# Optimization experiments

Measured on AMD Instinct MI355X. Metric: run time of the kernel, lower is better.

## Reference

```python
import jax, jax.numpy as jnp
import numpy as np

N_NODES = 100000   # total atoms across batch
N_EDGES = 1600000  # directed edges (avg degree 16)
ATOM_FDIM = 75
N_MOLS = 1024
DEPTH = 3


def setup_inputs() -> dict:
    key = jax.random.key(0)
    ks = jax.random.split(key, 8)
    h = jax.random.normal(ks[0], (N_NODES, ATOM_FDIM), dtype=jnp.float32)
    # U: Linear(2*atom_fdim -> atom_fdim); NN: Linear(atom_fdim -> 1)
    U_w = jax.random.normal(ks[1], (ATOM_FDIM, 2 * ATOM_FDIM), dtype=jnp.float32) * (1.0 / np.sqrt(2 * ATOM_FDIM))
    U_b = jnp.zeros((ATOM_FDIM,), dtype=jnp.float32)
    NN_w = jax.random.normal(ks[2], (1, ATOM_FDIM), dtype=jnp.float32) * (1.0 / np.sqrt(ATOM_FDIM))
    NN_b = jnp.zeros((1,), dtype=jnp.float32)
    edge_src = jax.random.randint(ks[3], (N_EDGES,), 0, N_NODES, dtype=jnp.int32)
    edge_dst = jax.random.randint(ks[4], (N_EDGES,), 0, N_NODES, dtype=jnp.int32)
    mol_id = jnp.sort(jax.random.randint(ks[5], (N_NODES,), 0, N_MOLS, dtype=jnp.int32))
    return {
        "h": h, "U_w": U_w, "U_b": U_b, "NN_w": NN_w, "NN_b": NN_b,
        "edge_src": edge_src, "edge_dst": edge_dst, "mol_id": mol_id,
        "depth": DEPTH, "num_mols": N_MOLS,
    }


def reference(h, U_w, U_b, NN_w, NN_b, edge_src, edge_dst, mol_id, depth, num_mols):
    n_nodes = h.shape[0]
    for _ in range(depth):
        # message: sum of neighbor atom features (gather + scatter-add)
        m = jax.ops.segment_sum(h[edge_src], edge_dst, num_segments=n_nodes)  # [N, D]
        # update: h_v = relu(U([h_v ; m_v]))
        h = jax.nn.relu(jnp.concatenate([h, m], axis=-1) @ U_w.T + U_b)
    # readout: sum atom vectors per molecule, then Linear(D -> 1)
    mol_vec = jax.ops.segment_sum(h, mol_id, num_segments=num_mols)  # [B, D]
    out = mol_vec @ NN_w.T + NN_b  # [B, 1]
    return out
```

## Files before the change

kernel.cpp:

```cpp
#include <hip/hip_runtime.h>

#define FDIM 75
#define CDIM 150
#define NSB 80
#define BW 7
#define BSZ (1 << BW)
#define TILE_E 4096
#define EPT 16

typedef __attribute__((ext_vector_type(8))) short bf16x8;
typedef __attribute__((ext_vector_type(4))) float f32x4;
typedef __attribute__((ext_vector_type(4))) int   i32x4;

__device__ __forceinline__ unsigned f2bf(float x) {
    unsigned u = __float_as_uint(x);
    return (u + 0x7FFFu + ((u >> 16) & 1u)) >> 16;
}
__device__ __forceinline__ float bf_lo(unsigned u) { return __uint_as_float(u << 16); }
__device__ __forceinline__ float bf_hi(unsigned u) { return __uint_as_float(u & 0xFFFF0000u); }

__global__ void pad_convert_kernel(const float* __restrict__ h_in,
                                   unsigned* __restrict__ h40, int n_nodes) {
    int i = blockIdx.x * blockDim.x + threadIdx.x;
    int total = n_nodes * 40;
    if (i >= total) return;
    int v = i / 40, d = i - v * 40;
    int f0 = 2 * d, f1 = 2 * d + 1;
    float a = (f0 < FDIM) ? h_in[(size_t)v * FDIM + f0] : 0.0f;
    float b = (f1 < FDIM) ? h_in[(size_t)v * FDIM + f1] : 0.0f;
    h40[i] = f2bf(a) | (f2bf(b) << 16);
}

__global__ void wprep_kernel(const float* __restrict__ Uw,
                             unsigned short* __restrict__ wpack) {
    int i = blockIdx.x * blockDim.x + threadIdx.x;
    if (i >= 1600) return;
    int kb = i / 80, c = i - kb * 80;
    unsigned short out[8];
#pragma unroll
    for (int j = 0; j < 8; ++j) {
        int k = kb * 8 + j;
        float v = 0.0f;
        if (c < FDIM) {
            if (k < FDIM)                 v = Uw[(size_t)c * CDIM + k];
            else if (k >= 80 && k < 155)  v = Uw[(size_t)c * CDIM + FDIM + (k - 80)];
        }
        out[j] = (unsigned short)f2bf(v);
    }
    *(i32x4*)&wpack[(size_t)i * 8] = *(i32x4*)out;
}

__global__ __launch_bounds__(256) void bcount_kernel(
        const int* __restrict__ edst, int* __restrict__ bcnt,
        int n_edges, int nb) {
    __shared__ int lh[1024];
    int tid = threadIdx.x;
    for (int i = tid; i < nb; i += 256) lh[i] = 0;
    __syncthreads();
    for (int e = blockIdx.x * blockDim.x + tid; e < n_edges;
         e += gridDim.x * blockDim.x)
        atomicAdd(&lh[edst[e] >> BW], 1);
    __syncthreads();
    for (int i = tid; i < nb; i += 256)
        if (lh[i]) atomicAdd(&bcnt[i], lh[i]);
}

__global__ __launch_bounds__(1024) void bscan_kernel(
        const int* __restrict__ bcnt, int* __restrict__ bbase,
        int* __restrict__ gcur, int* __restrict__ row_ptr,
        int nb, int n_nodes) {
    __shared__ int s[1024];
    int t = threadIdx.x;
    int v = (t < nb) ? bcnt[t] : 0;
    s[t] = v;
    __syncthreads();
    for (int off = 1; off < 1024; off <<= 1) {
        int x = (t >= off) ? s[t - off] : 0;
        __syncthreads();
        s[t] += x;
        __syncthreads();
    }
    if (t < nb) {
        int ex = s[t] - v;
        bbase[t] = ex;
        gcur[t] = ex;
    }
    if (t == nb - 1) {
        bbase[nb] = s[t];
        row_ptr[n_nodes] = s[t];
    }
}

__global__ __launch_bounds__(256) void bpart_kernel(
        const int* __restrict__ esrc, const int* __restrict__ edst,
        int* __restrict__ gcur, unsigned* __restrict__ pairs,
        int n_edges, int nb) {
    __shared__ int lh[1024];
    __shared__ int tbase[1024];
    int tid = threadIdx.x;
    int base = blockIdx.x * TILE_E;
    unsigned packedR[EPT];
    int bR[EPT];
    for (int i = tid; i < nb; i += 256) lh[i] = 0;
    __syncthreads();
#pragma unroll
    for (int k = 0; k < EPT; ++k) {
        int e = base + k * 256 + tid;
        if (e < n_edges) {
            int d = edst[e];
            int s = esrc[e];
            bR[k] = d >> BW;
            packedR[k] = ((unsigned)(d & (BSZ - 1)) << 17) | (unsigned)s;
            atomicAdd(&lh[bR[k]], 1);
        } else {
            bR[k] = -1;
        }
    }
    __syncthreads();
    for (int i = tid; i < nb; i += 256) {
        int c = lh[i];
        if (c) tbase[i] = atomicAdd(&gcur[i], c);
        lh[i] = 0;
    }
    __syncthreads();
#pragma unroll
    for (int k = 0; k < EPT; ++k) {
        if (bR[k] >= 0) {
            int off = atomicAdd(&lh[bR[k]], 1);
            pairs[tbase[bR[k]] + off] = packedR[k];
        }
    }
}

__global__ __launch_bounds__(256) void bfill_kernel(
        const unsigned* __restrict__ pairs, const int* __restrict__ bbase,
        int* __restrict__ row_ptr, int* __restrict__ csr, int n_nodes) {
    __shared__ int cnt[BSZ];
    __shared__ int ofs[BSZ];
    __shared__ int cur[BSZ];
    int b = blockIdx.x;
    int tid = threadIdx.x;
    int v0 = b << BW;
    int nbk = n_nodes - v0;
    if (nbk > BSZ) nbk = BSZ;
    int sbeg = bbase[b];
    int ne = bbase[b + 1] - sbeg;
    if (tid < BSZ) { cnt[tid] = 0; cur[tid] = 0; }
    __syncthreads();
    for (int i = tid; i < ne; i += 256)
        atomicAdd(&cnt[pairs[sbeg + i] >> 17], 1);
    __syncthreads();
    if (tid < BSZ) ofs[tid] = cnt[tid];
    __syncthreads();
    for (int off = 1; off < BSZ; off <<= 1) {
        int x = 0;
        if (tid < BSZ && tid >= off) x = ofs[tid - off];
        __syncthreads();
        if (tid < BSZ) ofs[tid] += x;
        __syncthreads();
    }
    if (tid < nbk) row_ptr[v0 + tid] = sbeg + ofs[tid] - cnt[tid];
    __syncthreads();
    for (int i = tid; i < ne; i += 256) {
        unsigned p = pairs[sbeg + i];
        int dl = p >> 17;
        int src = p & 0x1FFFF;
        int pos = (ofs[dl] - cnt[dl]) + atomicAdd(&cur[dl], 1);
        csr[sbeg + pos] = src;
    }
}

__global__ __launch_bounds__(256) void gather_kernel(
        const unsigned* __restrict__ h32, unsigned* __restrict__ m32,
        const int* __restrict__ row_ptr, const int* __restrict__ csr,
        int n_nodes) {
    int lane = threadIdx.x & 63;
    int wid = blockIdx.x * (blockDim.x >> 6) + (threadIdx.x >> 6);
    int nwaves = gridDim.x * (blockDim.x >> 6);
    bool act = (lane < 40);

    for (int v = wid; v < n_nodes; v += nwaves) {
        int e0 = row_ptr[v];
        int e1 = row_ptr[v + 1];
        float a0 = 0.f, a1 = 0.f, a2 = 0.f, a3 = 0.f;
        float c0 = 0.f, c1 = 0.f, c2 = 0.f, c3 = 0.f;
        int e = e0;
        while (e < e1) {
            int cnt = e1 - e;
            if (cnt > 64) cnt = 64;
            int myi = (lane < cnt) ? csr[e + lane] : 0;
            int d = 0;
            for (; d + 8 <= cnt; d += 8) {
                int s0 = __shfl(myi, d + 0);
                int s1 = __shfl(myi, d + 1);
                int s2 = __shfl(myi, d + 2);
                int s3 = __shfl(myi, d + 3);
                int s4 = __shfl(myi, d + 4);
                int s5 = __shfl(myi, d + 5);
                int s6 = __shfl(myi, d + 6);
                int s7 = __shfl(myi, d + 7);
                if (act) {
                    unsigned u0 = h32[(size_t)s0 * 40 + lane];
                    unsigned u1 = h32[(size_t)s1 * 40 + lane];
                    unsigned u2 = h32[(size_t)s2 * 40 + lane];
                    unsigned u3 = h32[(size_t)s3 * 40 + lane];
                    unsigned u4 = h32[(size_t)s4 * 40 + lane];
                    unsigned u5 = h32[(size_t)s5 * 40 + lane];
                    unsigned u6 = h32[(size_t)s6 * 40 + lane];
                    unsigned u7 = h32[(size_t)s7 * 40 + lane];
                    a0 += bf_lo(u0); c0 += bf_hi(u0);
                    a1 += bf_lo(u1); c1 += bf_hi(u1);
                    a2 += bf_lo(u2); c2 += bf_hi(u2);
                    a3 += bf_lo(u3); c3 += bf_hi(u3);
                    a0 += bf_lo(u4); c0 += bf_hi(u4);
                    a1 += bf_lo(u5); c1 += bf_hi(u5);
                    a2 += bf_lo(u6); c2 += bf_hi(u6);
                    a3 += bf_lo(u7); c3 += bf_hi(u7);
                }
            }
            for (; d + 4 <= cnt; d += 4) {
                int s0 = __shfl(myi, d + 0);
                int s1 = __shfl(myi, d + 1);
                int s2 = __shfl(myi, d + 2);
                int s3 = __shfl(myi, d + 3);
                if (act) {
                    unsigned u0 = h32[(size_t)s0 * 40 + lane];
                    unsigned u1 = h32[(size_t)s1 * 40 + lane];
                    unsigned u2 = h32[(size_t)s2 * 40 + lane];
                    unsigned u3 = h32[(size_t)s3 * 40 + lane];
                    a0 += bf_lo(u0); c0 += bf_hi(u0);
                    a1 += bf_lo(u1); c1 += bf_hi(u1);
                    a2 += bf_lo(u2); c2 += bf_hi(u2);
                    a3 += bf_lo(u3); c3 += bf_hi(u3);
                }
            }
            for (; d < cnt; ++d) {
                int s0 = __shfl(myi, d);
                if (act) {
                    unsigned u0 = h32[(size_t)s0 * 40 + lane];
                    a0 += bf_lo(u0); c0 += bf_hi(u0);
                }
            }
            e += cnt;
        }
        if (act) {
            float lo = (a0 + a1) + (a2 + a3);
            float hi = (c0 + c1) + (c2 + c3);
            m32[(size_t)v * 40 + lane] = f2bf(lo) | (f2bf(hi) << 16);
        }
    }
}

__global__ __launch_bounds__(256) void update_mfma_kernel(
        unsigned short* __restrict__ h, const unsigned short* __restrict__ m,
        const unsigned short* __restrict__ wpack, const float* __restrict__ Ub,
        int n_nodes) {
    __shared__ __align__(16) unsigned short Wl[12800];
    __shared__ __align__(16) unsigned short Xl[4][16][168];
    int tid = threadIdx.x;

    for (int i = tid; i < 1600; i += 256)
        *(i32x4*)&Wl[i * 8] = *(const i32x4*)&wpack[(size_t)i * 8];

    int base = blockIdx.x * 64;
    for (int i = tid; i < 64 * 20; i += 256) {
        int nl = i / 20, p = i - nl * 20;
        int v = base + nl;
        i32x4 val = {0, 0, 0, 0};
        if (v < n_nodes) {
            const unsigned short* src = (p < 10)
                ? h + (size_t)v * NSB + p * 8
                : m + (size_t)v * NSB + (p - 10) * 8;
            val = *(const i32x4*)src;
        }
        *(i32x4*)&Xl[nl >> 4][nl & 15][p * 8] = val;
    }
    __syncthreads();

    int w = tid >> 6;
    int lane = tid & 63;
    int col = lane & 15;
    int kb = lane >> 4;
    float bias[5];
#pragma unroll
    for (int jt = 0; jt < 5; ++jt) {
        int c = jt * 16 + col;
        bias[jt] = (c < FDIM) ? Ub[c] : 0.0f;
    }

    f32x4 acc[5] = {};
#pragma unroll
    for (int t = 0; t < 5; ++t) {
        bf16x8 a = *(bf16x8*)&Xl[w][col][t * 32 + kb * 8];
#pragma unroll
        for (int jt = 0; jt < 5; ++jt) {
            bf16x8 b = *(bf16x8*)&Wl[((t * 4 + kb) * 80 + jt * 16 + col) * 8];
            acc[jt] = __builtin_amdgcn_mfma_f32_16x16x32_bf16(a, b, acc[jt], 0, 0, 0);
        }
    }

#pragma unroll
    for (int jt = 0; jt < 5; ++jt) {
        int c = jt * 16 + col;
        if (c >= FDIM) continue;
#pragma unroll
        for (int r = 0; r < 4; ++r) {
            int node = base + w * 16 + kb * 4 + r;
            if (node < n_nodes) {
                float vv = fmaxf(acc[jt][r] + bias[jt], 0.0f);
                h[(size_t)node * NSB + c] = (unsigned short)f2bf(vv);
            }
        }
    }
}

__global__ __launch_bounds__(256) void readout_mol_kernel(
        const unsigned* __restrict__ h32, const float* __restrict__ NNw,
        const int* __restrict__ mol_id, const float* __restrict__ NN_b,
        float* __restrict__ out, int n_nodes) {
    int b = blockIdx.x;
    int lo = 0, hi = n_nodes;
    while (lo < hi) {
        int mid = (lo + hi) >> 1;
        if (mol_id[mid] < b) lo = mid + 1; else hi = mid;
    }
    int start = lo;
    hi = n_nodes;
    while (lo < hi) {
        int mid = (lo + hi) >> 1;
        if (mol_id[mid] < b + 1) lo = mid + 1; else hi = mid;
    }
    int end = lo;

    int tid = threadIdx.x;
    int wave = tid >> 6, lane = tid & 63;
    float w0 = 0.f, w1 = 0.f;
    if (lane < 40) {
        w0 = (2 * lane < FDIM) ? NNw[2 * lane] : 0.f;
        w1 = (2 * lane + 1 < FDIM) ? NNw[2 * lane + 1] : 0.f;
    }
    float wsum = 0.f;
    for (int v = start + wave; v < end; v += 4) {
        if (lane < 40) {
            unsigned u = h32[(size_t)v * 40 + lane];
            wsum += bf_lo(u) * w0 + bf_hi(u) * w1;
        }
    }
    wsum += __shfl_down(wsum, 32);
    wsum += __shfl_down(wsum, 16);
    wsum += __shfl_down(wsum, 8);
    wsum += __shfl_down(wsum, 4);
    wsum += __shfl_down(wsum, 2);
    wsum += __shfl_down(wsum, 1);
    __shared__ float part[4];
    if (lane == 0) part[wave] = wsum;
    __syncthreads();
    if (tid == 0) out[b] = NN_b[0] + part[0] + part[1] + part[2] + part[3];
}

extern "C" void kernel_launch(void* const* d_in, const int* in_sizes, int n_in,
                              void* d_out, int out_size, void* d_ws, size_t ws_size,
                              hipStream_t stream) {
    const float* h_src = (const float*)d_in[0];
    const float* U_w   = (const float*)d_in[1];
    const float* U_b   = (const float*)d_in[2];
    const float* NN_w  = (const float*)d_in[3];
    const float* NN_b  = (const float*)d_in[4];
    const int*   esrc  = (const int*)d_in[5];
    const int*   edst  = (const int*)d_in[6];
    const int*   molid = (const int*)d_in[7];

    int n_nodes  = in_sizes[0] / FDIM;
    int n_edges  = in_sizes[5];
    int num_mols = out_size;
    const int depth = 3;
    int nb = (n_nodes + BSZ - 1) >> BW;

    size_t row_bytes = (size_t)n_nodes * NSB * sizeof(unsigned short);

    size_t off = 0;
    auto alloc = [&](size_t bytes) {
        size_t o = off;
        off += (bytes + 255) & ~(size_t)255;
        return o;
    };
    char* ws = (char*)d_ws;
    size_t o_h     = alloc(row_bytes);
    size_t o_m     = alloc(row_bytes);
    size_t o_rp    = alloc(((size_t)n_nodes + 1) * sizeof(int));
    size_t o_csr   = alloc((size_t)n_edges * sizeof(int));
    size_t o_wp    = alloc(12800 * sizeof(unsigned short));
    size_t o_bcnt  = alloc((size_t)(nb + 1) * sizeof(int));
    size_t o_bbase = alloc((size_t)(nb + 1) * sizeof(int));
    size_t o_gcur  = alloc((size_t)(nb + 1) * sizeof(int));
    (void)ws_size;

    float* out = (float*)d_out;
    unsigned short* h = (unsigned short*)(ws + o_h);
    unsigned short* m = (unsigned short*)(ws + o_m);
    unsigned* pairs = (unsigned*)(ws + o_m);
    int* row_ptr = (int*)(ws + o_rp);
    int* csr     = (int*)(ws + o_csr);
    unsigned short* wpack = (unsigned short*)(ws + o_wp);
    int* bcnt    = (int*)(ws + o_bcnt);
    int* bbase   = (int*)(ws + o_bbase);
    int* gcur    = (int*)(ws + o_gcur);

    pad_convert_kernel<<<(n_nodes * 40 + 255) / 256, 256, 0, stream>>>(
        h_src, (unsigned*)h, n_nodes);
    wprep_kernel<<<7, 256, 0, stream>>>(U_w, wpack);

    hipMemsetAsync(bcnt, 0, (size_t)nb * sizeof(int), stream);
    bcount_kernel<<<256, 256, 0, stream>>>(edst, bcnt, n_edges, nb);
    bscan_kernel<<<1, 1024, 0, stream>>>(bcnt, bbase, gcur, row_ptr, nb, n_nodes);
    bpart_kernel<<<(n_edges + TILE_E - 1) / TILE_E, 256, 0, stream>>>(
        esrc, edst, gcur, pairs, n_edges, nb);
    bfill_kernel<<<nb, 256, 0, stream>>>(pairs, bbase, row_ptr, csr, n_nodes);

    int ublocks = (n_nodes + 63) / 64;
    for (int d = 0; d < depth; ++d) {
        gather_kernel<<<2048, 256, 0, stream>>>(
            (const unsigned*)h, (unsigned*)m, row_ptr, csr, n_nodes);
        update_mfma_kernel<<<ublocks, 256, 0, stream>>>(h, m, wpack, U_b, n_nodes);
    }

    readout_mol_kernel<<<num_mols, 256, 0, stream>>>(
        (const unsigned*)h, NN_w, molid, NN_b, out, n_nodes);
}
```

Before: 305.0 us.

## Fuse neighbor gather and MFMA update into one per-depth kernel with ping-pong buffers

Merges the gather and update kernels into a single kernel per depth. Each wave sums the neighbors of 16 nodes directly into shared memory and then runs the MFMA update, so the message buffer m no longer makes a round trip through global memory. Ping-pong h buffers are used because other blocks still read the input features. The weights are now read from global memory instead of being staged in LDS. The risk is load imbalance from the fixed 16-nodes-per-wave assignment and less latency hiding than the grid-stride gather had.

```diff
diff --git a/kernel.cpp b/kernel.cpp
--- a/kernel.cpp
+++ b/kernel.cpp
@@ -170,145 +170,120 @@
     }
 }
 
-__global__ __launch_bounds__(256) void gather_kernel(
-        const unsigned* __restrict__ h32, unsigned* __restrict__ m32,
+__global__ __launch_bounds__(256) void depth_fused_kernel(
+        const unsigned* __restrict__ hin32,
+        unsigned short* __restrict__ hout,
         const int* __restrict__ row_ptr, const int* __restrict__ csr,
-        int n_nodes) {
-    int lane = threadIdx.x & 63;
-    int wid = blockIdx.x * (blockDim.x >> 6) + (threadIdx.x >> 6);
-    int nwaves = gridDim.x * (blockDim.x >> 6);
-    bool act = (lane < 40);
-
-    for (int v = wid; v < n_nodes; v += nwaves) {
-        int e0 = row_ptr[v];
-        int e1 = row_ptr[v + 1];
-        float a0 = 0.f, a1 = 0.f, a2 = 0.f, a3 = 0.f;
-        float c0 = 0.f, c1 = 0.f, c2 = 0.f, c3 = 0.f;
-        int e = e0;
-        while (e < e1) {
-            int cnt = e1 - e;
-            if (cnt > 64) cnt = 64;
-            int myi = (lane < cnt) ? csr[e + lane] : 0;
-            int d = 0;
-            for (; d + 8 <= cnt; d += 8) {
-                int s0 = __shfl(myi, d + 0);
-                int s1 = __shfl(myi, d + 1);
-                int s2 = __shfl(myi, d + 2);
-                int s3 = __shfl(myi, d + 3);
-                int s4 = __shfl(myi, d + 4);
-                int s5 = __shfl(myi, d + 5);
-                int s6 = __shfl(myi, d + 6);
-                int s7 = __shfl(myi, d + 7);
-                if (act) {
-                    unsigned u0 = h32[(size_t)s0 * 40 + lane];
-                    unsigned u1 = h32[(size_t)s1 * 40 + lane];
-                    unsigned u2 = h32[(size_t)s2 * 40 + lane];
-                    unsigned u3 = h32[(size_t)s3 * 40 + lane];
-                    unsigned u4 = h32[(size_t)s4 * 40 + lane];
-                    unsigned u5 = h32[(size_t)s5 * 40 + lane];
-                    unsigned u6 = h32[(size_t)s6 * 40 + lane];
-                    unsigned u7 = h32[(size_t)s7 * 40 + lane];
-                    a0 += bf_lo(u0); c0 += bf_hi(u0);
-                    a1 += bf_lo(u1); c1 += bf_hi(u1);
-                    a2 += bf_lo(u2); c2 += bf_hi(u2);
-                    a3 += bf_lo(u3); c3 += bf_hi(u3);
-                    a0 += bf_lo(u4); c0 += bf_hi(u4);
-                    a1 += bf_lo(u5); c1 += bf_hi(u5);
-                    a2 += bf_lo(u6); c2 += bf_hi(u6);
-                    a3 += bf_lo(u7); c3 += bf_hi(u7);
-                }
-            }
-            for (; d + 4 <= cnt; d += 4) {
-                int s0 = __shfl(myi, d + 0);
-                int s1 = __shfl(myi, d + 1);
-                int s2 = __shfl(myi, d + 2);
-                int s3 = __shfl(myi, d + 3);
-                if (act) {
-                    unsigned u0 = h32[(size_t)s0 * 40 + lane];
-                    unsigned u1 = h32[(size_t)s1 * 40 + lane];
-                    unsigned u2 = h32[(size_t)s2 * 40 + lane];
-                    unsigned u3 = h32[(size_t)s3 * 40 + lane];
-                    a0 += bf_lo(u0); c0 += bf_hi(u0);
-                    a1 += bf_lo(u1); c1 += bf_hi(u1);
-                    a2 += bf_lo(u2); c2 += bf_hi(u2);
-                    a3 += bf_lo(u3); c3 += bf_hi(u3);
-                }
-            }
-            for (; d < cnt; ++d) {
-                int s0 = __shfl(myi, d);
-                if (act) {
-                    unsigned u0 = h32[(size_t)s0 * 40 + lane];
-                    a0 += bf_lo(u0); c0 += bf_hi(u0);
-                }
-            }
-            e += cnt;
-        }
-        if (act) {
-            float lo = (a0 + a1) + (a2 + a3);
-            float hi = (c0 + c1) + (c2 + c3);
-            m32[(size_t)v * 40 + lane] = f2bf(lo) | (f2bf(hi) << 16);
-        }
-    }
-}
-
-__global__ __launch_bounds__(256) void update_mfma_kernel(
-        unsigned short* __restrict__ h, const unsigned short* __restrict__ m,
         const unsigned short* __restrict__ wpack, const float* __restrict__ Ub,
         int n_nodes) {
-    __shared__ __align__(16) unsigned short Wl[12800];
     __shared__ __align__(16) unsigned short Xl[4][16][168];
     int tid = threadIdx.x;
-
-    for (int i = tid; i < 1600; i += 256)
-        *(i32x4*)&Wl[i * 8] = *(const i32x4*)&wpack[(size_t)i * 8];
-
+    int w = tid >> 6, lane = tid & 63;
     int base = blockIdx.x * 64;
-    for (int i = tid; i < 64 * 20; i += 256) {
-        int nl = i / 20, p = i - nl * 20;
-        int v = base + nl;
-        i32x4 val = {0, 0, 0, 0};
+    bool act = (lane < 40);
+
+    for (int i = 0; i < 16; ++i) {
+        int v = base + w * 16 + i;
         if (v < n_nodes) {
-            const unsigned short* src = (p < 10)
-                ? h + (size_t)v * NSB + p * 8
-                : m + (size_t)v * NSB + (p - 10) * 8;
-            val = *(const i32x4*)src;
-        }
-        *(i32x4*)&Xl[nl >> 4][nl & 15][p * 8] = val;
-    }
-    __syncthreads();
-
-    int w = tid >> 6;
-    int lane = tid & 63;
+            unsigned hv = act ? hin32[(size_t)v * 40 + lane] : 0u;
+            int e0 = row_ptr[v], e1 = row_ptr[v + 1];
+            float a0 = 0.f, a1 = 0.f, a2 = 0.f, a3 = 0.f;
+            float c0 = 0.f, c1 = 0.f, c2 = 0.f, c3 = 0.f;
+            int e = e0;
+            while (e < e1) {
+                int cnt = e1 - e;
+                if (cnt > 64) cnt = 64;
+                int myi = (lane < cnt) ? csr[e + lane] : 0;
+                int d = 0;
+                for (; d + 8 <= cnt; d += 8) {
+                    int s0 = __shfl(myi, d + 0);
+                    int s1 = __shfl(myi, d + 1);
+                    int s2 = __shfl(myi, d + 2);
+                    int s3 = __shfl(myi, d + 3);
+                    int s4 = __shfl(myi, d + 4);
+                    int s5 = __shfl(myi, d + 5);
+                    int s6 = __shfl(myi, d + 6);
+                    int s7 = __shfl(myi, d + 7);
+                    if (act) {
+                        unsigned u0 = hin32[(size_t)s0 * 40 + lane];
+                        unsigned u1 = hin32[(size_t)s1 * 40 + lane];
+                        unsigned u2 = hin32[(size_t)s2 * 40 + lane];
+                        unsigned u3 = hin32[(size_t)s3 * 40 + lane];
+                        unsigned u4 = hin32[(size_t)s4 * 40 + lane];
+                        unsigned u5 = hin32[(size_t)s5 * 40 + lane];
+                        unsigned u6 = hin32[(size_t)s6 * 40 + lane];
+                        unsigned u7 = hin32[(size_t)s7 * 40 + lane];
+                        a0 += bf_lo(u0); c0 += bf_hi(u0);
+                        a1 += bf_lo(u1); c1 += bf_hi(u1);
+                        a2 += bf_lo(u2); c2 += bf_hi(u2);
+                        a3 += bf_lo(u3); c3 += bf_hi(u3);
+                        a0 += bf_lo(u4); c0 += bf_hi(u4);
+                        a1 += bf_lo(u5); c1 += bf_hi(u5);
+                        a2 += bf_lo(u6); c2 += bf_hi(u6);
+                        a3 += bf_lo(u7); c3 += bf_hi(u7);
+                    }
+                }
+                for (; d + 4 <= cnt; d += 4) {
+                    int s0 = __shfl(myi, d + 0);
+                    int s1 = __shfl(myi, d + 1);
+                    int s2 = __shfl(myi, d + 2);
+                    int s3 = __shfl(myi, d + 3);
+                    if (act) {
+                        unsigned u0 = hin32[(size_t)s0 * 40 + lane];
+                        unsigned u1 = hin32[(size_t)s1 * 40 + lane];
+                        unsigned u2 = hin32[(size_t)s2 * 40 + lane];
+                        unsigned u3 = hin32[(size_t)s3 * 40 + lane];
+                        a0 += bf_lo(u0); c0 += bf_hi(u0);
+                        a1 += bf_lo(u1); c1 += bf_hi(u1);
+                        a2 += bf_lo(u2); c2 += bf_hi(u2);
+                        a3 += bf_lo(u3); c3 += bf_hi(u3);
+                    }
+                }
+                for (; d < cnt; ++d) {
+                    int s0 = __shfl(myi, d);
+                    if (act) {
+                        unsigned u0 = hin32[(size_t)s0 * 40 + lane];
+                        a0 += bf_lo(u0); c0 += bf_hi(u0);
+                    }
+                }
+                e += cnt;
+            }
+            if (act) {
+                *(unsigned*)&Xl[w][i][2 * lane] = hv;
+                float lo = (a0 + a1) + (a2 + a3);
+                float hi = (c0 + c1) + (c2 + c3);
+                *(unsigned*)&Xl[w][i][80 + 2 * lane] = f2bf(lo) | (f2bf(hi) << 16);
+            }
+        } else if (act) {
+            *(unsigned*)&Xl[w][i][2 * lane] = 0u;
+            *(unsigned*)&Xl[w][i][80 + 2 * lane] = 0u;
+        }
+    }
+    __syncthreads();
+
     int col = lane & 15;
     int kb = lane >> 4;
-    float bias[5];
+    f32x4 acc[5] = {};
+#pragma unroll
+    for (int t = 0; t < 5; ++t) {
+        bf16x8 a = *(bf16x8*)&Xl[w][col][t * 32 + kb * 8];
+#pragma unroll
+        for (int jt = 0; jt < 5; ++jt) {
+            bf16x8 b = *(const bf16x8*)&wpack[((size_t)((t * 4 + kb) * 80 + jt * 16 + col)) * 8];
+            acc[jt] = __builtin_amdgcn_mfma_f32_16x16x32_bf16(a, b, acc[jt], 0, 0, 0);
+        }
+    }
+
 #pragma unroll
     for (int jt = 0; jt < 5; ++jt) {
         int c = jt * 16 + col;
-        bias[jt] = (c < FDIM) ? Ub[c] : 0.0f;
-    }
-
-    f32x4 acc[5] = {};
-#pragma unroll
-    for (int t = 0; t < 5; ++t) {
-        bf16x8 a = *(bf16x8*)&Xl[w][col][t * 32 + kb * 8];
-#pragma unroll
-        for (int jt = 0; jt < 5; ++jt) {
-            bf16x8 b = *(bf16x8*)&Wl[((t * 4 + kb) * 80 + jt * 16 + col) * 8];
-            acc[jt] = __builtin_amdgcn_mfma_f32_16x16x32_bf16(a, b, acc[jt], 0, 0, 0);
-        }
-    }
-
-#pragma unroll
-    for (int jt = 0; jt < 5; ++jt) {
-        int c = jt * 16 + col;
-        if (c >= FDIM) continue;
+        float bj = (c < FDIM) ? Ub[c] : 0.0f;
 #pragma unroll
         for (int r = 0; r < 4; ++r) {
             int node = base + w * 16 + kb * 4 + r;
             if (node < n_nodes) {
-                float vv = fmaxf(acc[jt][r] + bias[jt], 0.0f);
-                h[(size_t)node * NSB + c] = (unsigned short)f2bf(vv);
+                float vv = fmaxf(acc[jt][r] + bj, 0.0f);
+                hout[(size_t)node * NSB + c] = (unsigned short)f2bf(vv);
             }
         }
     }
@@ -385,8 +360,8 @@
         return o;
     };
     char* ws = (char*)d_ws;
-    size_t o_h     = alloc(row_bytes);
-    size_t o_m     = alloc(row_bytes);
+    size_t o_hA    = alloc(row_bytes);
+    size_t o_hB    = alloc(row_bytes);
     size_t o_rp    = alloc(((size_t)n_nodes + 1) * sizeof(int));
     size_t o_csr   = alloc((size_t)n_edges * sizeof(int));
     size_t o_wp    = alloc(12800 * sizeof(unsigned short));
@@ -396,9 +371,9 @@
     (void)ws_size;
 
     float* out = (float*)d_out;
-    unsigned short* h = (unsigned short*)(ws + o_h);
-    unsigned short* m = (unsigned short*)(ws + o_m);
-    unsigned* pairs = (unsigned*)(ws + o_m);
+    unsigned short* hA = (unsigned short*)(ws + o_hA);
+    unsigned short* hB = (unsigned short*)(ws + o_hB);
+    unsigned* pairs = (unsigned*)(ws + o_hB);
     int* row_ptr = (int*)(ws + o_rp);
     int* csr     = (int*)(ws + o_csr);
     unsigned short* wpack = (unsigned short*)(ws + o_wp);
@@ -407,7 +382,7 @@
     int* gcur    = (int*)(ws + o_gcur);
 
     pad_convert_kernel<<<(n_nodes * 40 + 255) / 256, 256, 0, stream>>>(
-        h_src, (unsigned*)h, n_nodes);
+        h_src, (unsigned*)hA, n_nodes);
     wprep_kernel<<<7, 256, 0, stream>>>(U_w, wpack);
 
     hipMemsetAsync(bcnt, 0, (size_t)nb * sizeof(int), stream);
@@ -418,12 +393,16 @@
     bfill_kernel<<<nb, 256, 0, stream>>>(pairs, bbase, row_ptr, csr, n_nodes);
 
     int ublocks = (n_nodes + 63) / 64;
+    const unsigned short* hin = hA;
+    unsigned short* hout = hB;
     for (int d = 0; d < depth; ++d) {
-        gather_kernel<<<2048, 256, 0, stream>>>(
-            (const unsigned*)h, (unsigned*)m, row_ptr, csr, n_nodes);
-        update_mfma_kernel<<<ublocks, 256, 0, stream>>>(h, m, wpack, U_b, n_nodes);
+        depth_fused_kernel<<<ublocks, 256, 0, stream>>>(
+            (const unsigned*)hin, hout, row_ptr, csr, wpack, U_b, n_nodes);
+        const unsigned short* t = hout;
+        hout = (unsigned short*)hin;
+        hin = t;
     }
 
     readout_mol_kernel<<<num_mols, 256, 0, stream>>>(
-        (const unsigned*)h, NN_w, molid, NN_b, out, n_nodes);
-}
+        (const unsigned*)hin, NN_w, molid, NN_b, out, n_nodes);
+}
```

New measurement: 374.2 us. 1.23x slower.
